# Optimization experiments

Measured on AMD Instinct MI355X. Metric: run time of the kernel, lower is better.

The kernel has to match this reference:

```python
import jax, jax.numpy as jnp
import numpy as np

BS, NE, NN, CIN, H, D = 8, 4800, 4981, 3, 128, 6
EPG = 19200
NEDGE = BS * EPG
N = BS * NE

PARAM_NAMES = [
    'enc_cw1','enc_cb1','enc_cw2','enc_cb2','enc_cw3','enc_clng','enc_clnb',
    'enc_ew1','enc_eb1','enc_ew2','enc_eb2','enc_ew3','enc_elng','enc_elnb',
    'p_ew1','p_eb1','p_ew2','p_eb2','p_ew3','p_elng','p_elnb',
    'p_nw1','p_nb1','p_nw2','p_nb2','p_nw3','p_nlng','p_nlnb',
    'dec_uw1','dec_ub1','dec_uw2','dec_ub2','dec_uw3','dec_ulng','dec_ulnb',
    'dec_cw1','dec_cb1','dec_cw2','dec_cb2','dec_cw3']


def setup_inputs():
    key = jax.random.key(0)
    ks = iter(jax.random.split(key, 64))
    def nrm(shape, s=0.1):
        return jax.random.normal(next(ks), shape, jnp.float32) * s
    inp = {}
    inp['x'] = jax.random.normal(next(ks), (BS * NN, CIN), jnp.float32)
    inp['elem_conn'] = jax.random.randint(next(ks), (NE, 4), 0, NN)
    inp['edge_index'] = jax.random.randint(next(ks), (2, NEDGE), 0, N)
    inp['enc_cw1'] = nrm((CIN, 4, 1)); inp['enc_cb1'] = nrm((CIN, 1), 0.01)
    inp['enc_cw2'] = nrm((CIN, 1, 1)); inp['enc_cb2'] = nrm((CIN, 1), 0.01)
    inp['enc_cw3'] = nrm((CIN, 1, 1))
    inp['enc_clng'] = jnp.ones((CIN, 1)); inp['enc_clnb'] = jnp.zeros((CIN, 1))
    inp['enc_ew1'] = nrm((CIN, H)); inp['enc_eb1'] = nrm((H,), 0.01)
    inp['enc_ew2'] = nrm((H, H)); inp['enc_eb2'] = nrm((H,), 0.01)
    inp['enc_ew3'] = nrm((H, H))
    inp['enc_elng'] = jnp.ones((H,)); inp['enc_elnb'] = jnp.zeros((H,))
    inp['p_ew1'] = nrm((D, 2 * H, H)); inp['p_eb1'] = nrm((D, H), 0.01)
    inp['p_ew2'] = nrm((D, H, H)); inp['p_eb2'] = nrm((D, H), 0.01)
    inp['p_ew3'] = nrm((D, H, H))
    inp['p_elng'] = jnp.ones((D, H)); inp['p_elnb'] = jnp.zeros((D, H))
    inp['p_nw1'] = nrm((D, 2 * H, H)); inp['p_nb1'] = nrm((D, H), 0.01)
    inp['p_nw2'] = nrm((D, H, H)); inp['p_nb2'] = nrm((D, H), 0.01)
    inp['p_nw3'] = nrm((D, H, H))
    inp['p_nlng'] = jnp.ones((D, H)); inp['p_nlnb'] = jnp.zeros((D, H))
    inp['dec_uw1'] = nrm((H, 1, 4)); inp['dec_ub1'] = nrm((H, 4), 0.01)
    inp['dec_uw2'] = nrm((H, 4, 4)); inp['dec_ub2'] = nrm((H, 4), 0.01)
    inp['dec_uw3'] = nrm((H, 4, 4))
    inp['dec_ulng'] = jnp.ones((H, 4)); inp['dec_ulnb'] = jnp.zeros((H, 4))
    inp['dec_cw1'] = nrm((H, CIN)); inp['dec_cb1'] = nrm((CIN,), 0.01)
    inp['dec_cw2'] = nrm((CIN, CIN)); inp['dec_cb2'] = nrm((CIN,), 0.01)
    inp['dec_cw3'] = nrm((CIN, CIN))
    return inp


def lrelu(x):
    return jnp.where(x >= 0, x, 0.2 * x)


def ln(x, g, b, axis=-1):
    m = jnp.mean(x, axis=axis, keepdims=True)
    v = jnp.var(x, axis=axis, keepdims=True)
    return (x - m) / jnp.sqrt(v + 1e-5) * g + b


def mlp(x, w1, b1, w2, b2, w3):
    h = lrelu(x @ w1 + b1)
    h = lrelu(h @ w2 + b2)
    return h @ w3


def _forward(fl, elem_conn, edge_index):
    x = fl[0]
    P = dict(zip(PARAM_NAMES, fl[1:]))
    # ---- Encoder: MeshCNN gather (4 mesh nodes per element) + per-channel MLP 4->1 ----
    xg = x.reshape(BS, NN, CIN)[:, elem_conn]                  # (BS, NE, 4, CIN)
    h = lrelu(jnp.einsum('beic,cio->beoc', xg, P['enc_cw1']) + P['enc_cb1'].T[None, None])
    h = lrelu(jnp.einsum('beic,cio->beoc', h, P['enc_cw2']) + P['enc_cb2'].T[None, None])
    h = jnp.einsum('beic,cio->beoc', h, P['enc_cw3'])
    h = ln(h, P['enc_clng'].T[None, None], P['enc_clnb'].T[None, None], axis=2)  # LayerNorm(1)
    h = h[:, :, 0, :].reshape(N, CIN)
    h = ln(mlp(h, P['enc_ew1'], P['enc_eb1'], P['enc_ew2'], P['enc_eb2'], P['enc_ew3']),
           P['enc_elng'], P['enc_elnb'])                       # (N, H)
    # ---- Processor: D GraphNet blocks, edge MLP + scatter-add + node MLP ----
    src, dest = edge_index[0], edge_index[1]
    stacked = (P['p_ew1'], P['p_eb1'], P['p_ew2'], P['p_eb2'], P['p_ew3'], P['p_elng'], P['p_elnb'],
               P['p_nw1'], P['p_nb1'], P['p_nw2'], P['p_nb2'], P['p_nw3'], P['p_nlng'], P['p_nlnb'])
    def step(hc, p):
        ew1, eb1, ew2, eb2, ew3, eg, ebv, nw1, nb1, nw2, nb2, nw3, ng, nbv = p
        msg = jnp.concatenate([hc[dest], hc[src]], axis=-1)    # (NEDGE, 2H)
        m = ln(mlp(msg, ew1, eb1, ew2, eb2, ew3), eg, ebv)
        aggr = jax.ops.segment_sum(m, dest, num_segments=N)
        hn = ln(mlp(jnp.concatenate([hc, aggr], axis=-1), nw1, nb1, nw2, nb2, nw3), ng, nbv)
        return hn, None
    h, _ = jax.lax.scan(step, h, stacked)
    # ---- Decoder: per-channel upsample 1->4 then index_add back to mesh nodes ----
    u = h.reshape(BS, NE, H)[:, :, None, :]                    # (BS, NE, 1, H)
    u = lrelu(jnp.einsum('beic,cio->beoc', u, P['dec_uw1']) + P['dec_ub1'].T[None, None])
    u = lrelu(jnp.einsum('beic,cio->beoc', u, P['dec_uw2']) + P['dec_ub2'].T[None, None])
    u = jnp.einsum('beic,cio->beoc', u, P['dec_uw3'])
    u = ln(u, P['dec_ulng'].T[None, None], P['dec_ulnb'].T[None, None], axis=2)  # (BS, NE, 4, H)
    out = jnp.zeros((BS, NN, H), u.dtype).at[:, elem_conn.reshape(-1)].add(u.reshape(BS, NE * 4, H))
    out = out.reshape(BS * NN, H)
    o = lrelu(out @ P['dec_cw1'] + P['dec_cb1'])
    o = lrelu(o @ P['dec_cw2'] + P['dec_cb2'])
    return o @ P['dec_cw3']


def reference(x, elem_conn, edge_index,
              enc_cw1, enc_cb1, enc_cw2, enc_cb2, enc_cw3, enc_clng, enc_clnb,
              enc_ew1, enc_eb1, enc_ew2, enc_eb2, enc_ew3, enc_elng, enc_elnb,
              p_ew1, p_eb1, p_ew2, p_eb2, p_ew3, p_elng, p_elnb,
              p_nw1, p_nb1, p_nw2, p_nb2, p_nw3, p_nlng, p_nlnb,
              dec_uw1, dec_ub1, dec_uw2, dec_ub2, dec_uw3, dec_ulng, dec_ulnb,
              dec_cw1, dec_cb1, dec_cw2, dec_cb2, dec_cw3):
    fl = (x, enc_cw1, enc_cb1, enc_cw2, enc_cb2, enc_cw3, enc_clng, enc_clnb,
          enc_ew1, enc_eb1, enc_ew2, enc_eb2, enc_ew3, enc_elng, enc_elnb,
          p_ew1, p_eb1, p_ew2, p_eb2, p_ew3, p_elng, p_elnb,
          p_nw1, p_nb1, p_nw2, p_nb2, p_nw3, p_nlng, p_nlnb,
          dec_uw1, dec_ub1, dec_uw2, dec_ub2, dec_uw3, dec_ulng, dec_ulnb,
          dec_cw1, dec_cb1, dec_cw2, dec_cb2, dec_cw3)
    return _forward(fl, elem_conn, edge_index)
```

## Files before the change

kernel.cpp:

```cpp
#include <hip/hip_runtime.h>
#include <hip/hip_fp16.h>
#include <math.h>

#define BS    8
#define NE    4800
#define NN    4981
#define CIN   3
#define HD    128
#define DBLK  6
#define NEDGE 153600
#define NTOT  38400
#define NMESH (BS*NN)
#define NNP   5120
#define EM    128

#define UW1T  0
#define UB1T  512
#define UW2T  1024
#define UB2T  3072
#define UW3T  3584
#define ULNGT 5632
#define ULNBT 6144
#define DWT_N 6656

typedef _Float16 f16;
typedef _Float16 f16x8 __attribute__((ext_vector_type(8)));
typedef float f32x4 __attribute__((ext_vector_type(4)));

__device__ __forceinline__ float lrelu(float x) { return x >= 0.0f ? x : 0.2f * x; }

__global__ __launch_bounds__(128)
void enc_msg0_kernel(const float* __restrict__ clnb,
                     const float* __restrict__ ew1, const float* __restrict__ eb1,
                     const float* __restrict__ ew2, const float* __restrict__ eb2,
                     const float* __restrict__ ew3,
                     const float* __restrict__ g, const float* __restrict__ b,
                     float* __restrict__ hv0,
                     const float* __restrict__ pew1, const float* __restrict__ peb1,
                     const float* __restrict__ pew2, const float* __restrict__ peb2,
                     const float* __restrict__ pew3,
                     const float* __restrict__ pg, const float* __restrict__ pb,
                     float* __restrict__ m0) {
    __shared__ float s1[HD], s2[HD], s3[HD], hv[HD];
    int j = threadIdx.x;
    float a = eb1[j];
    for (int c = 0; c < CIN; ++c) a += clnb[c] * ew1[c * HD + j];
    s1[j] = lrelu(a);
    __syncthreads();
    a = eb2[j];
    for (int k = 0; k < HD; ++k) a += s1[k] * ew2[k * HD + j];
    s2[j] = lrelu(a);
    __syncthreads();
    a = 0.0f;
    for (int k = 0; k < HD; ++k) a += s2[k] * ew3[k * HD + j];
    s3[j] = a;
    __syncthreads();
    float m = 0.0f;
    for (int k = 0; k < HD; ++k) m += s3[k];
    m *= (1.0f / HD);
    float v = 0.0f;
    for (int k = 0; k < HD; ++k) { float d = s3[k] - m; v += d * d; }
    v *= (1.0f / HD);
    float rs = 1.0f / sqrtf(v + 1e-5f);
    float h0 = (s3[j] - m) * rs * g[j] + b[j];
    hv0[j] = h0;
    hv[j] = h0;
    __syncthreads();
    a = peb1[j];
    for (int k = 0; k < HD; ++k) a += hv[k] * (pew1[k * HD + j] + pew1[(k + HD) * HD + j]);
    s1[j] = lrelu(a);
    __syncthreads();
    a = peb2[j];
    for (int k = 0; k < HD; ++k) a += s1[k] * pew2[k * HD + j];
    s2[j] = lrelu(a);
    __syncthreads();
    a = 0.0f;
    for (int k = 0; k < HD; ++k) a += s2[k] * pew3[k * HD + j];
    s3[j] = a;
    __syncthreads();
    m = 0.0f;
    for (int k = 0; k < HD; ++k) m += s3[k];
    m *= (1.0f / HD);
    v = 0.0f;
    for (int k = 0; k < HD; ++k) { float d = s3[k] - m; v += d * d; }
    v *= (1.0f / HD);
    rs = 1.0f / sqrtf(v + 1e-5f);
    m0[j] = (s3[j] - m) * rs * pg[j] + pb[j];
}

__global__ __launch_bounds__(256)
void conv_all_kernel(const float* __restrict__ ew1, const float* __restrict__ ew2,
                     const float* __restrict__ ew3,
                     const float* __restrict__ nw1, const float* __restrict__ nw2,
                     const float* __restrict__ nw3, f16* __restrict__ wbuf,
                     const float* __restrict__ eb1, f16* __restrict__ eb16,
                     const float* __restrict__ uw1, const float* __restrict__ ub1,
                     const float* __restrict__ uw2, const float* __restrict__ ub2,
                     const float* __restrict__ uw3, const float* __restrict__ ulng,
                     const float* __restrict__ ulnb, float* __restrict__ dwt) {
    int b = blockIdx.x;
    int tid = threadIdx.x;
    if (b == 48) {
        for (int i = tid; i < DBLK * HD; i += 256)
            eb16[i] = (f16)eb1[i];
        return;
    }
    if (b == 49) {
        for (int idx = tid; idx < 512; idx += 256) {
            int o = idx >> 7, c = idx & 127;
            dwt[UW1T + idx] = uw1[c * 4 + o];
            dwt[UB1T + idx] = ub1[c * 4 + o];
            dwt[UB2T + idx] = ub2[c * 4 + o];
            dwt[ULNGT + idx] = ulng[c * 4 + o];
            dwt[ULNBT + idx] = ulnb[c * 4 + o];
        }
        for (int idx = tid; idx < 2048; idx += 256) {
            int io = idx >> 7, c = idx & 127;
            dwt[UW2T + idx] = uw2[c * 16 + io];
            dwt[UW3T + idx] = uw3[c * 16 + io];
        }
        return;
    }
    int d = b >> 3, m = b & 7;
    const float* src;
    switch (m) {
        case 0: src = ew1 + (size_t)d * 2 * HD * HD; break;
        case 1: src = ew1 + (size_t)d * 2 * HD * HD + HD * HD; break;
        case 2: src = ew2 + (size_t)d * HD * HD; break;
        case 3: src = ew3 + (size_t)d * HD * HD; break;
        case 4: src = nw1 + (size_t)d * 2 * HD * HD; break;
        case 5: src = nw1 + (size_t)d * 2 * HD * HD + HD * HD; break;
        case 6: src = nw2 + (size_t)d * HD * HD; break;
        default: src = nw3 + (size_t)d * HD * HD; break;
    }
    f16* out = wbuf + (size_t)b * HD * HD;
    for (int idx = tid; idx < HD * HD; idx += 256) {
        int n = idx >> 7, k = idx & 127;
        out[idx] = (f16)src[k * HD + n];
    }
}

#define EHB (NEDGE / 256)
#define MHB (NE * 4 / 256)
#define ESB (NTOT / 256)
#define MSB (NNP / 256)

__global__ __launch_bounds__(256)
void prep_hist(const int* __restrict__ e_dst, const int* __restrict__ conn,
               int* __restrict__ deg, int* __restrict__ mdeg) {
    int b = blockIdx.x;
    if (b < EHB) {
        int e = b * 256 + threadIdx.x;
        atomicAdd(&deg[e_dst[e]], 1);
    } else {
        int idx = (b - EHB) * 256 + threadIdx.x;
        atomicAdd(&mdeg[conn[idx]], 1);
    }
}

__device__ __forceinline__ void scan1_body(const int* __restrict__ deg,
                                           int* __restrict__ rowptr,
                                           int* __restrict__ bsum, int bi) {
    __shared__ int s[256];
    int i = bi * 256 + threadIdx.x;
    int v = deg[i];
    s[threadIdx.x] = v;
    __syncthreads();
    for (int off = 1; off < 256; off <<= 1) {
        int t = (threadIdx.x >= off) ? s[threadIdx.x - off] : 0;
        __syncthreads();
        s[threadIdx.x] += t;
        __syncthreads();
    }
    rowptr[i] = s[threadIdx.x] - v;
    if (threadIdx.x == 255) bsum[bi] = s[255];
}

__global__ __launch_bounds__(256)
void prep_scan1(const int* __restrict__ deg, int* __restrict__ rowptr,
                int* __restrict__ bsum,
                const int* __restrict__ mdeg, int* __restrict__ mrow,
                int* __restrict__ mbsum) {
    int b = blockIdx.x;
    if (b < ESB) scan1_body(deg, rowptr, bsum, b);
    else         scan1_body(mdeg, mrow, mbsum, b - ESB);
}

__device__ __forceinline__ void scan2_body(int* __restrict__ bsum, int nb) {
    __shared__ int s[256];
    int v = (threadIdx.x < nb) ? bsum[threadIdx.x] : 0;
    s[threadIdx.x] = v;
    __syncthreads();
    for (int off = 1; off < 256; off <<= 1) {
        int t = (threadIdx.x >= off) ? s[threadIdx.x - off] : 0;
        __syncthreads();
        s[threadIdx.x] += t;
        __syncthreads();
    }
    if (threadIdx.x < nb) bsum[threadIdx.x] = s[threadIdx.x] - v;
}

__global__ __launch_bounds__(256)
void prep_scan2(int* __restrict__ bsum, int* __restrict__ mbsum) {
    if (blockIdx.x == 0) scan2_body(bsum, ESB);
    else                 scan2_body(mbsum, MSB);
}

__global__ __launch_bounds__(256)
void prep_scan3(int* __restrict__ rowptr, const int* __restrict__ bsum,
                int* __restrict__ mrow, const int* __restrict__ mbsum) {
    int b = blockIdx.x;
    if (b < ESB) {
        int i = b * 256 + threadIdx.x;
        rowptr[i] += bsum[b];
    } else {
        int i = (b - ESB) * 256 + threadIdx.x;
        mrow[i] += mbsum[b - ESB];
    }
}

__global__ __launch_bounds__(256)
void prep_scatter(const int* __restrict__ dest, const int* __restrict__ srcv,
                  const int* __restrict__ rowptr, int* __restrict__ cursor,
                  int* __restrict__ dsorted, int* __restrict__ ssorted,
                  const int* __restrict__ conn, const int* __restrict__ mrow,
                  int* __restrict__ mcur, int* __restrict__ mslot) {
    int b = blockIdx.x;
    if (b < EHB) {
        int e = b * 256 + threadIdx.x;
        int d = dest[e];
        int pos = rowptr[d] + atomicAdd(&cursor[d], 1);
        dsorted[pos] = d;
        ssorted[pos] = srcv[e];
    } else {
        int idx = (b - EHB) * 256 + threadIdx.x;
        int nd = conn[idx];
        int pos = mrow[nd] + atomicAdd(&mcur[nd], 1);
        mslot[pos] = idx;
    }
}

template <int NT>
__device__ __forceinline__ void stage_w(const f16* __restrict__ Wg, f16 (*Bt)[HD + 8],
                                        int tid) {
    #pragma unroll
    for (int t = 0; t < 2048 / NT; ++t) {
        int idx = tid + t * NT;
        int r = idx >> 4, c = (idx & 15) * 8;
        *(uint4*)(&Bt[r][c]) = *(const uint4*)(Wg + (size_t)r * HD + c);
    }
}

__device__ __forceinline__ void mfma_pass(const f16 (*A)[HD + 8], const f16 (*Bt)[HD + 8],
                                          int rt_base, int ct_base, int ln, int quad,
                                          f32x4 acc[2][4]) {
    #pragma unroll
    for (int ks = 0; ks < 4; ++ks) {
        int kb = ks * 32 + quad * 8;
        f16x8 a0 = *(const f16x8*)(&A[rt_base + ln][kb]);
        f16x8 a1 = *(const f16x8*)(&A[rt_base + 16 + ln][kb]);
        #pragma unroll
        for (int c = 0; c < 4; ++c) {
            f16x8 b = *(const f16x8*)(&Bt[ct_base + c * 16 + ln][kb]);
            acc[0][c] = __builtin_amdgcn_mfma_f32_16x16x32_f16(a0, b, acc[0][c], 0, 0, 0);
            acc[1][c] = __builtin_amdgcn_mfma_f32_16x16x32_f16(a1, b, acc[1][c], 0, 0, 0);
        }
    }
}

__global__ __launch_bounds__(512, 4)
void gn_edge(const f16* __restrict__ P1, const f16* __restrict__ P2,
             const int* __restrict__ dsorted, const int* __restrict__ ssorted,
             const f16* __restrict__ W2, const f16* __restrict__ W3,
             const f16* __restrict__ b1h, const float* __restrict__ b2,
             const float* __restrict__ g, const float* __restrict__ bln,
             f16* __restrict__ msg) {
    __shared__ __align__(16) f16 As[EM][HD + 8];
    __shared__ __align__(16) f16 Bt[HD][HD + 8];
    __shared__ float red[EM][2][2];

    const int tid = threadIdx.x;
    const int base = blockIdx.x * EM;
    const int wave = tid >> 6, lane = tid & 63;
    const int ln = lane & 15, quad = lane >> 4;
    const int rt_base = (wave >> 1) * 32;
    const int ct_base = (wave & 1) * 64;
    const int half = wave & 1;
    const int r0 = tid >> 4;
    const int cg = (tid & 15) * 8;

    const f16 k02s = (f16)0.2f;
    const f16x8 k02 = {k02s, k02s, k02s, k02s, k02s, k02s, k02s, k02s};

    int dI[4], sI[4];
    #pragma unroll
    for (int it = 0; it < 4; ++it) {
        dI[it] = dsorted[base + r0 + it * 32];
        sI[it] = ssorted[base + r0 + it * 32];
    }
    stage_w<512>(W2, Bt, tid);
    const f16x8 bb = *(const f16x8*)(b1h + cg);
    #pragma unroll
    for (int it = 0; it < 4; ++it) {
        f16x8 p1 = *(const f16x8*)(P1 + (size_t)dI[it] * HD + cg);
        f16x8 p2 = *(const f16x8*)(P2 + (size_t)sI[it] * HD + cg);
        f16x8 s = p1 + p2 + bb;
        *(f16x8*)(&As[r0 + it * 32][cg]) = __builtin_elementwise_max(s, s * k02);
    }
    __syncthreads();

    f32x4 acc[2][4];

    #pragma unroll
    for (int c = 0; c < 4; ++c) {
        float bj = b2[ct_base + c * 16 + ln];
        f32x4 bv = {bj, bj, bj, bj};
        acc[0][c] = bv; acc[1][c] = bv;
    }
    mfma_pass(As, Bt, rt_base, ct_base, ln, quad, acc);
    __syncthreads();
    stage_w<512>(W3, Bt, tid);
    #pragma unroll
    for (int i = 0; i < 2; ++i)
        #pragma unroll
        for (int c = 0; c < 4; ++c)
            #pragma unroll
            for (int r = 0; r < 4; ++r)
                As[rt_base + i * 16 + quad * 4 + r][ct_base + c * 16 + ln] =
                    (f16)lrelu(acc[i][c][r]);
    __syncthreads();

    #pragma unroll
    for (int c = 0; c < 4; ++c) { f32x4 z = {0,0,0,0}; acc[0][c] = z; acc[1][c] = z; }
    mfma_pass(As, Bt, rt_base, ct_base, ln, quad, acc);

    #pragma unroll
    for (int i = 0; i < 2; ++i)
        #pragma unroll
        for (int r = 0; r < 4; ++r) {
            float s = acc[i][0][r] + acc[i][1][r] + acc[i][2][r] + acc[i][3][r];
            float q = acc[i][0][r] * acc[i][0][r] + acc[i][1][r] * acc[i][1][r] +
                      acc[i][2][r] * acc[i][2][r] + acc[i][3][r] * acc[i][3][r];
            s += __shfl_xor(s, 1); q += __shfl_xor(q, 1);
            s += __shfl_xor(s, 2); q += __shfl_xor(q, 2);
            s += __shfl_xor(s, 4); q += __shfl_xor(q, 4);
            s += __shfl_xor(s, 8); q += __shfl_xor(q, 8);
            if (ln == 0) {
                int row = rt_base + i * 16 + quad * 4 + r;
                red[row][half][0] = s;
                red[row][half][1] = q;
            }
        }
    __syncthreads();

    float gv[4], bv[4];
    #pragma unroll
    for (int c = 0; c < 4; ++c) {
        int col = ct_base + c * 16 + ln;
        gv[c] = g[col]; bv[c] = bln[col];
    }
    #pragma unroll
    for (int i = 0; i < 2; ++i)
        #pragma unroll
        for (int r = 0; r < 4; ++r) {
            int row = rt_base + i * 16 + quad * 4 + r;
            float s = red[row][0][0] + red[row][1][0];
            float q = red[row][0][1] + red[row][1][1];
            float m = s * (1.0f / HD);
            float var = q * (1.0f / HD) - m * m;
            float rs = 1.0f / sqrtf(var + 1e-5f);
            #pragma unroll
            for (int c = 0; c < 4; ++c) {
                int col = ct_base + c * 16 + ln;
                float v = (acc[i][c][r] - m) * rs * gv[c] + bv[c];
                msg[(size_t)(base + row) * HD + col] = (f16)v;
            }
        }
}

template <int AGGR, bool PROD, bool DECF>
__global__ __launch_bounds__(256, 3)
void gn_node(f16* __restrict__ h16, const f16* __restrict__ msg,
             const int* __restrict__ rowptr, const int* __restrict__ deg,
             const float* __restrict__ m0, const float* __restrict__ hv0,
             const f16* __restrict__ W1a, const f16* __restrict__ W1b,
             const f16* __restrict__ W2, const f16* __restrict__ W3,
             const float* __restrict__ b1, const float* __restrict__ b2,
             const float* __restrict__ g, const float* __restrict__ bln,
             const f16* __restrict__ nW1a, const f16* __restrict__ nW1b,
             f16* __restrict__ P1, f16* __restrict__ P2,
             const float* __restrict__ dwt, f16* __restrict__ uval) {
    __shared__ __align__(16) f16 As[64][HD + 8];
    __shared__ __align__(16) f16 Bt[HD][HD + 8];
    __shared__ float red[64][2][2];

    const int tid = threadIdx.x;
    const int base = blockIdx.x * 64;
    const int wave = tid >> 6, lane = tid & 63;
    const int ln = lane & 15, quad = lane >> 4;
    const int rt_base = (wave >> 1) * 32;
    const int ct_base = (wave & 1) * 64;
    const int half = wave & 1;

    f16x8 hreg[4];
    #pragma unroll
    for (int t = 0; t < 4; ++t) {
        int r = (tid >> 4) + t * 16;
        int c = (tid & 15) * 8;
        if (AGGR == 0) {
            f16x8 hz;
            #pragma unroll
            for (int u = 0; u < 8; ++u) hz[u] = (f16)hv0[c + u];
            hreg[t] = hz;
            float sc = (float)deg[base + r];
            f16x8 o;
            #pragma unroll
            for (int u = 0; u < 8; ++u) o[u] = (f16)(sc * m0[c + u]);
            *(f16x8*)(&As[r][c]) = o;
        } else {
            hreg[t] = *(const f16x8*)(h16 + (size_t)(base + r) * HD + c);
            int rp = rowptr[base + r], dg = deg[base + r];
            float a[8] = {0, 0, 0, 0, 0, 0, 0, 0};
            int j = 0;
            for (; j + 4 <= dg; j += 4) {
                f16x8 v0 = *(const f16x8*)(msg + (size_t)(rp + j) * HD + c);
                f16x8 v1 = *(const f16x8*)(msg + (size_t)(rp + j + 1) * HD + c);
                f16x8 v2 = *(const f16x8*)(msg + (size_t)(rp + j + 2) * HD + c);
                f16x8 v3 = *(const f16x8*)(msg + (size_t)(rp + j + 3) * HD + c);
                #pragma unroll
                for (int u = 0; u < 8; ++u)
                    a[u] += ((float)v0[u] + (float)v1[u]) + ((float)v2[u] + (float)v3[u]);
            }
            for (; j < dg; ++j) {
                f16x8 mv = *(const f16x8*)(msg + (size_t)(rp + j) * HD + c);
                #pragma unroll
                for (int u = 0; u < 8; ++u) a[u] += (float)mv[u];
            }
            f16x8 o;
            #pragma unroll
            for (int u = 0; u < 8; ++u) o[u] = (f16)a[u];
            *(f16x8*)(&As[r][c]) = o;
        }
    }
    stage_w<256>(W1b, Bt, tid);
    __syncthreads();

    f32x4 acc[2][4];
    #pragma unroll
    for (int c = 0; c < 4; ++c) {
        float bj = b1[ct_base + c * 16 + ln];
        f32x4 bb = {bj, bj, bj, bj};
        acc[0][c] = bb; acc[1][c] = bb;
    }
    mfma_pass(As, Bt, rt_base, ct_base, ln, quad, acc);
    __syncthreads();

    #pragma unroll
    for (int t = 0; t < 4; ++t) {
        int r = (tid >> 4) + t * 16;
        int c = (tid & 15) * 8;
        *(f16x8*)(&As[r][c]) = hreg[t];
    }
    stage_w<256>(W1a, Bt, tid);
    __syncthreads();
    mfma_pass(As, Bt, rt_base, ct_base, ln, quad, acc);
    __syncthreads();

    stage_w<256>(W2, Bt, tid);
    #pragma unroll
    for (int i = 0; i < 2; ++i)
        #pragma unroll
        for (int c = 0; c < 4; ++c)
            #pragma unroll
            for (int r = 0; r < 4; ++r)
                As[rt_base + i * 16 + quad * 4 + r][ct_base + c * 16 + ln] =
                    (f16)lrelu(acc[i][c][r]);
    __syncthreads();

    #pragma unroll
    for (int c = 0; c < 4; ++c) {
        float bj = b2[ct_base + c * 16 + ln];
        f32x4 bb = {bj, bj, bj, bj};
        acc[0][c] = bb; acc[1][c] = bb;
    }
    mfma_pass(As, Bt, rt_base, ct_base, ln, quad, acc);
    __syncthreads();
    stage_w<256>(W3, Bt, tid);
    #pragma unroll
    for (int i = 0; i < 2; ++i)
        #pragma unroll
        for (int c = 0; c < 4; ++c)
            #pragma unroll
            for (int r = 0; r < 4; ++r)
                As[rt_base + i * 16 + quad * 4 + r][ct_base + c * 16 + ln] =
                    (f16)lrelu(acc[i][c][r]);
    __syncthreads();

    #pragma unroll
    for (int c = 0; c < 4; ++c) { f32x4 z = {0,0,0,0}; acc[0][c] = z; acc[1][c] = z; }
    mfma_pass(As, Bt, rt_base, ct_base, ln, quad, acc);

    #pragma unroll
    for (int i = 0; i < 2; ++i)
        #pragma unroll
        for (int r = 0; r < 4; ++r) {
            float s = acc[i][0][r] + acc[i][1][r] + acc[i][2][r] + acc[i][3][r];
            float q = acc[i][0][r] * acc[i][0][r] + acc[i][1][r] * acc[i][1][r] +
                      acc[i][2][r] * acc[i][2][r] + acc[i][3][r] * acc[i][3][r];
            s += __shfl_xor(s, 1); q += __shfl_xor(q, 1);
            s += __shfl_xor(s, 2); q += __shfl_xor(q, 2);
            s += __shfl_xor(s, 4); q += __shfl_xor(q, 4);
            s += __shfl_xor(s, 8); q += __shfl_xor(q, 8);
            if (ln == 0) {
                int row = rt_base + i * 16 + quad * 4 + r;
                red[row][half][0] = s;
                red[row][half][1] = q;
            }
        }
    __syncthreads();

    float gv[4], bv[4];
    #pragma unroll
    for (int c = 0; c < 4; ++c) {
        int col = ct_base + c * 16 + ln;
        gv[c] = g[col]; bv[c] = bln[col];
    }

    if (!DECF) {
        #pragma unroll
        for (int i = 0; i < 2; ++i)
            #pragma unroll
            for (int r = 0; r < 4; ++r) {
                int row = rt_base + i * 16 + quad * 4 + r;
                float s = red[row][0][0] + red[row][1][0];
                float q = red[row][0][1] + red[row][1][1];
                float m = s * (1.0f / HD);
                float var = q * (1.0f / HD) - m * m;
                float rs = 1.0f / sqrtf(var + 1e-5f);
                #pragma unroll
                for (int c = 0; c < 4; ++c) {
                    int col = ct_base + c * 16 + ln;
                    float v = (acc[i][c][r] - m) * rs * gv[c] + bv[c];
                    f16 hv = (f16)v;
                    h16[(size_t)(base + row) * HD + col] = hv;
                    if (PROD) As[row][col] = hv;
                }
            }
    } else {
        float mm[2][4], rr[2][4];
        #pragma unroll
        for (int i = 0; i < 2; ++i)
            #pragma unroll
            for (int r = 0; r < 4; ++r) {
                int row = rt_base + i * 16 + quad * 4 + r;
                float s = red[row][0][0] + red[row][1][0];
                float q = red[row][0][1] + red[row][1][1];
                float m = s * (1.0f / HD);
                float var = q * (1.0f / HD) - m * m;
                mm[i][r] = m;
                rr[i][r] = 1.0f / sqrtf(var + 1e-5f);
            }
        #pragma unroll
        for (int c = 0; c < 4; ++c) {
            int col = ct_base + c * 16 + ln;
            float w1v[4], wb1[4], wb2[4], lg4[4], lb4[4];
            #pragma unroll
            for (int o = 0; o < 4; ++o) {
                w1v[o] = dwt[UW1T + o * 128 + col];
                wb1[o] = dwt[UB1T + o * 128 + col];
                wb2[o] = dwt[UB2T + o * 128 + col];
                lg4[o] = dwt[ULNGT + o * 128 + col];
                lb4[o] = dwt[ULNBT + o * 128 + col];
            }
            float w2v[16], w3v[16];
            #pragma unroll
            for (int io = 0; io < 16; ++io) {
                w2v[io] = dwt[UW2T + io * 128 + col];
                w3v[io] = dwt[UW3T + io * 128 + col];
            }
            #pragma unroll
            for (int i = 0; i < 2; ++i)
                #pragma unroll
                for (int r = 0; r < 4; ++r) {
                    int row = rt_base + i * 16 + quad * 4 + r;
                    float v = (acc[i][c][r] - mm[i][r]) * rr[i][r] * gv[c] + bv[c];
                    float s = (float)(f16)v;
                    float u1[4], u2[4], u3[4];
                    #pragma unroll
                    for (int o = 0; o < 4; ++o)
                        u1[o] = lrelu(s * w1v[o] + wb1[o]);
                    #pragma unroll
                    for (int o = 0; o < 4; ++o) {
                        float a = wb2[o];
                        #pragma unroll
                        for (int i2 = 0; i2 < 4; ++i2) a += u1[i2] * w2v[i2 * 4 + o];
                        u2[o] = lrelu(a);
                    }
                    #pragma unroll
                    for (int o = 0; o < 4; ++o) {
                        float a = 0.f;
                        #pragma unroll
                        for (int i2 = 0; i2 < 4; ++i2) a += u2[i2] * w3v[i2 * 4 + o];
                        u3[o] = a;
                    }
                    float m4 = 0.25f * (u3[0] + u3[1] + u3[2] + u3[3]);
                    float var4 = 0.f;
                    #pragma unroll
                    for (int o = 0; o < 4; ++o) { float d = u3[o] - m4; var4 += d * d; }
                    var4 *= 0.25f;
                    float rs4 = 1.0f / sqrtf(var4 + 1e-5f);
                    size_t ub = (size_t)(base + row) * 4 * HD + col;
                    #pragma unroll
                    for (int o = 0; o < 4; ++o)
                        uval[ub + (size_t)o * HD] =
                            (f16)((u3[o] - m4) * rs4 * lg4[o] + lb4[o]);
                }
        }
    }

    if (PROD) {
        __syncthreads();
        stage_w<256>(nW1a, Bt, tid);
        __syncthreads();
        #pragma unroll
        for (int c = 0; c < 4; ++c) { f32x4 z = {0,0,0,0}; acc[0][c] = z; acc[1][c] = z; }
        mfma_pass(As, Bt, rt_base, ct_base, ln, quad, acc);
        #pragma unroll
        for (int i = 0; i < 2; ++i)
            #pragma unroll
            for (int c = 0; c < 4; ++c)
                #pragma unroll
                for (int r = 0; r < 4; ++r)
                    P1[(size_t)(base + rt_base + i * 16 + quad * 4 + r) * HD +
                       ct_base + c * 16 + ln] = (f16)acc[i][c][r];
        __syncthreads();
        stage_w<256>(nW1b, Bt, tid);
        __syncthreads();
        #pragma unroll
        for (int c = 0; c < 4; ++c) { f32x4 z = {0,0,0,0}; acc[0][c] = z; acc[1][c] = z; }
        mfma_pass(As, Bt, rt_base, ct_base, ln, quad, acc);
        #pragma unroll
        for (int i = 0; i < 2; ++i)
            #pragma unroll
            for (int c = 0; c < 4; ++c)
                #pragma unroll
                for (int r = 0; r < 4; ++r)
                    P2[(size_t)(base + rt_base + i * 16 + quad * 4 + r) * HD +
                       ct_base + c * 16 + ln] = (f16)acc[i][c][r];
    }
}

__global__ __launch_bounds__(256)
void dec_gather_out(const f16* __restrict__ uval,
                    const int* __restrict__ mrow, const int* __restrict__ mdeg,
                    const int* __restrict__ mslot,
                    const float* __restrict__ cw1, const float* __restrict__ cb1,
                    const float* __restrict__ cw2, const float* __restrict__ cb2,
                    const float* __restrict__ cw3,
                    float* __restrict__ o, int nrows) {
    int r = blockIdx.x * 4 + (threadIdx.x >> 6);
    if (r >= nrows) return;
    int lane = threadIdx.x & 63;
    int b = r / NN, n = r - b * NN;
    int rp = mrow[n], dg = mdeg[n];
    size_t boff = (size_t)b * NE * 4;
    float a0 = 0.f, a1 = 0.f;
    int j = 0;
    for (; j + 4 <= dg; j += 4) {
        int s0 = mslot[rp + j], s1 = mslot[rp + j + 1];
        int s2 = mslot[rp + j + 2], s3 = mslot[rp + j + 3];
        const f16* u0 = uval + (boff + s0) * HD + lane * 2;
        const f16* u1 = uval + (boff + s1) * HD + lane * 2;
        const f16* u2 = uval + (boff + s2) * HD + lane * 2;
        const f16* u3 = uval + (boff + s3) * HD + lane * 2;
        float b00 = (float)u0[0], b01 = (float)u0[1];
        float b10 = (float)u1[0], b11 = (float)u1[1];
        float b20 = (float)u2[0], b21 = (float)u2[1];
        float b30 = (float)u3[0], b31 = (float)u3[1];
        a0 += (b00 + b10) + (b20 + b30);
        a1 += (b01 + b11) + (b21 + b31);
    }
    for (; j < dg; ++j) {
        int slot = mslot[rp + j];
        const f16* up = uval + (boff + slot) * HD + lane * 2;
        a0 += (float)up[0];
        a1 += (float)up[1];
    }
    int c0 = lane * 2, c1 = lane * 2 + 1;
    float s[3];
    #pragma unroll
    for (int k = 0; k < 3; ++k)
        s[k] = a0 * cw1[c0 * 3 + k] + a1 * cw1[c1 * 3 + k];
    #pragma unroll
    for (int off = 32; off >= 1; off >>= 1) {
        s[0] += __shfl_down(s[0], off);
        s[1] += __shfl_down(s[1], off);
        s[2] += __shfl_down(s[2], off);
    }
    if (lane == 0) {
        float t1[3], t2[3];
        #pragma unroll
        for (int k = 0; k < 3; ++k) t1[k] = lrelu(s[k] + cb1[k]);
        #pragma unroll
        for (int k = 0; k < 3; ++k) {
            float a = cb2[k];
            #pragma unroll
            for (int q = 0; q < 3; ++q) a += t1[q] * cw2[q * 3 + k];
            t2[k] = lrelu(a);
        }
        #pragma unroll
        for (int k = 0; k < 3; ++k) {
            float a = 0.f;
            #pragma unroll
            for (int q = 0; q < 3; ++q) a += t2[q] * cw3[q * 3 + k];
            o[(size_t)r * 3 + k] = a;
        }
    }
}

extern "C" void kernel_launch(void* const* d_in, const int* in_sizes, int n_in,
                              void* d_out, int out_size, void* d_ws, size_t ws_size,
                              hipStream_t stream) {
    const int* elem_conn = (const int*)d_in[1];
    const int* edge_index = (const int*)d_in[2];
    const int* e_src = edge_index;
    const int* e_dst = edge_index + NEDGE;
    const float* enc_clnb = (const float*)d_in[9];
    const float* enc_ew1 = (const float*)d_in[10];
    const float* enc_eb1 = (const float*)d_in[11];
    const float* enc_ew2 = (const float*)d_in[12];
    const float* enc_eb2 = (const float*)d_in[13];
    const float* enc_ew3 = (const float*)d_in[14];
    const float* enc_elng = (const float*)d_in[15];
    const float* enc_elnb = (const float*)d_in[16];
    const float* p_ew1 = (const float*)d_in[17];
    const float* p_eb1 = (const float*)d_in[18];
    const float* p_ew2 = (const float*)d_in[19];
    const float* p_eb2 = (const float*)d_in[20];
    const float* p_ew3 = (const float*)d_in[21];
    const float* p_elng = (const float*)d_in[22];
    const float* p_elnb = (const float*)d_in[23];
    const float* p_nw1 = (const float*)d_in[24];
    const float* p_nb1 = (const float*)d_in[25];
    const float* p_nw2 = (const float*)d_in[26];
    const float* p_nb2 = (const float*)d_in[27];
    const float* p_nw3 = (const float*)d_in[28];
    const float* p_nlng = (const float*)d_in[29];
    const float* p_nlnb = (const float*)d_in[30];
    const float* dec_uw1 = (const float*)d_in[31];
    const float* dec_ub1 = (const float*)d_in[32];
    const float* dec_uw2 = (const float*)d_in[33];
    const float* dec_ub2 = (const float*)d_in[34];
    const float* dec_uw3 = (const float*)d_in[35];
    const float* dec_ulng = (const float*)d_in[36];
    const float* dec_ulnb = (const float*)d_in[37];
    const float* dec_cw1 = (const float*)d_in[38];
    const float* dec_cb1 = (const float*)d_in[39];
    const float* dec_cw2 = (const float*)d_in[40];
    const float* dec_cb2 = (const float*)d_in[41];
    const float* dec_cw3 = (const float*)d_in[42];

    char* ws = (char*)d_ws;
    f16*   h16     = (f16*)(ws);
    f16*   wbuf    = (f16*)(ws + 9830400);
    float* hv0     = (float*)(ws + 11403264);
    float* m0      = (float*)(ws + 11403776);
    f16*   P1      = (f16*)(ws + 11404288);
    f16*   P2      = (f16*)(ws + 21234688);
    f16*   msg     = (f16*)(ws + 31065088);
    int*   deg     = (int*)(ws + 70386688);
    int*   rowptr  = (int*)(ws + 70540288);
    int*   cursor  = (int*)(ws + 70693888);
    int*   bsum    = (int*)(ws + 70847488);
    int*   dsorted = (int*)(ws + 70848512);
    int*   ssorted = (int*)(ws + 71462912);
    f16*   eb16    = (f16*)(ws + 72077312);
    int*   mdeg    = (int*)(ws + 72078848);
    int*   mrow    = (int*)(ws + 72099328);
    int*   mcur    = (int*)(ws + 72119808);
    int*   mbsum   = (int*)(ws + 72140288);
    int*   mslot   = (int*)(ws + 72141312);
    float* dwt     = (float*)(ws + 72218112);
    f16*   uval    = (f16*)(ws + 72244736);

    hipMemsetAsync(deg, 0, 72218112 - 70386688, stream);

    enc_msg0_kernel<<<1, 128, 0, stream>>>(
        enc_clnb, enc_ew1, enc_eb1, enc_ew2, enc_eb2, enc_ew3, enc_elng, enc_elnb, hv0,
        p_ew1, p_eb1, p_ew2, p_eb2, p_ew3, p_elng, p_elnb, m0);
    conv_all_kernel<<<50, 256, 0, stream>>>(p_ew1, p_ew2, p_ew3,
                                            p_nw1, p_nw2, p_nw3, wbuf, p_eb1, eb16,
                                            dec_uw1, dec_ub1, dec_uw2, dec_ub2,
                                            dec_uw3, dec_ulng, dec_ulnb, dwt);

    prep_hist<<<EHB + MHB, 256, 0, stream>>>(e_dst, elem_conn, deg, mdeg);
    prep_scan1<<<ESB + MSB, 256, 0, stream>>>(deg, rowptr, bsum, mdeg, mrow, mbsum);
    prep_scan2<<<2, 256, 0, stream>>>(bsum, mbsum);
    prep_scan3<<<ESB + MSB, 256, 0, stream>>>(rowptr, bsum, mrow, mbsum);
    prep_scatter<<<EHB + MHB, 256, 0, stream>>>(e_dst, e_src, rowptr, cursor,
                                                dsorted, ssorted,
                                                elem_conn, mrow, mcur, mslot);

    {
        const f16* wd = wbuf;
        const f16* wn = wbuf + (size_t)8 * HD * HD;
        gn_node<0, true, false><<<NTOT / 64, 256, 0, stream>>>(
            h16, nullptr, nullptr, deg, m0, hv0,
            wd + 4 * HD * HD, wd + 5 * HD * HD, wd + 6 * HD * HD, wd + 7 * HD * HD,
            p_nb1, p_nb2, p_nlng, p_nlnb,
            wn + 0 * HD * HD, wn + 1 * HD * HD, P1, P2, nullptr, nullptr);
    }

    for (int d = 1; d < DBLK; ++d) {
        const f16* wd = wbuf + (size_t)d * 8 * HD * HD;
        gn_edge<<<NEDGE / EM, 512, 0, stream>>>(
            P1, P2, dsorted, ssorted,
            wd + 2 * HD * HD, wd + 3 * HD * HD,
            eb16 + (size_t)d * HD, p_eb2 + (size_t)d * HD,
            p_elng + (size_t)d * HD, p_elnb + (size_t)d * HD, msg);
        if (d < DBLK - 1) {
            const f16* wn = wbuf + (size_t)(d + 1) * 8 * HD * HD;
            gn_node<1, true, false><<<NTOT / 64, 256, 0, stream>>>(
                h16, msg, rowptr, deg, nullptr, nullptr,
                wd + 4 * HD * HD, wd + 5 * HD * HD, wd + 6 * HD * HD, wd + 7 * HD * HD,
                p_nb1 + (size_t)d * HD, p_nb2 + (size_t)d * HD,
                p_nlng + (size_t)d * HD, p_nlnb + (size_t)d * HD,
                wn + 0 * HD * HD, wn + 1 * HD * HD, P1, P2, nullptr, nullptr);
        } else {
            gn_node<1, false, true><<<NTOT / 64, 256, 0, stream>>>(
                h16, msg, rowptr, deg, nullptr, nullptr,
                wd + 4 * HD * HD, wd + 5 * HD * HD, wd + 6 * HD * HD, wd + 7 * HD * HD,
                p_nb1 + (size_t)d * HD, p_nb2 + (size_t)d * HD,
                p_nlng + (size_t)d * HD, p_nlnb + (size_t)d * HD,
                wbuf, wbuf, P1, P2, dwt, uval);
        }
    }

    dec_gather_out<<<(NMESH + 3) / 4, 256, 0, stream>>>(
        uval, mrow, mdeg, mslot, dec_cw1, dec_cb1, dec_cw2, dec_cb2, dec_cw3,
        (float*)d_out, NMESH);
}
```

Measured before the change: 578.4 us.

## Tabulate first GN node block by degree and prefetch node weights into registers

The first node block's inputs depend only on node in-degree, so its output is computed once for degrees 0..255 into small tables (h, P1, P2). The first edge block then gathers by per-edge degree, and the next node block reads h by degree, which removes a full-size node pass. The change also replaces the memset with zeroing blocks inside the conversion kernel, prefetches next-layer W1a/W1b into registers to overlap with the epilogue, and stages the decoder weights in shared memory. It assumes in-degree never exceeds 255, which holds for these random inputs but is not guaranteed in general, and the prefetch raises register pressure.

After: 629.8 us. +8.9%, slower.

```diff
diff --git a/kernel.cpp b/kernel.cpp
--- a/kernel.cpp
+++ b/kernel.cpp
@@ -13,6 +13,7 @@
 #define NMESH (BS*NN)
 #define NNP   5120
 #define EM    128
+#define TROWS 256
 
 #define UW1T  0
 #define UB1T  512
@@ -97,7 +98,9 @@
                      const float* __restrict__ uw1, const float* __restrict__ ub1,
                      const float* __restrict__ uw2, const float* __restrict__ ub2,
                      const float* __restrict__ uw3, const float* __restrict__ ulng,
-                     const float* __restrict__ ulnb, float* __restrict__ dwt) {
+                     const float* __restrict__ ulnb, float* __restrict__ dwt,
+                     int* __restrict__ zeroA, int* __restrict__ zeroB,
+                     int* __restrict__ degIota) {
     int b = blockIdx.x;
     int tid = threadIdx.x;
     if (b == 48) {
@@ -119,6 +122,19 @@
             dwt[UW2T + idx] = uw2[c * 16 + io];
             dwt[UW3T + idx] = uw3[c * 16 + io];
         }
+        return;
+    }
+    if (b >= 50 && b < 64) {
+        uint4 z = {0, 0, 0, 0};
+        for (int idx = (b - 50) * 256 + tid; idx < 28864; idx += 14 * 256)
+            ((uint4*)zeroA)[idx] = z;
+        return;
+    }
+    if (b == 64) {
+        uint4 z = {0, 0, 0, 0};
+        for (int idx = tid; idx < 3904; idx += 256)
+            ((uint4*)zeroB)[idx] = z;
+        degIota[tid] = tid;
         return;
     }
     int d = b >> 3, m = b & 7;
@@ -224,14 +240,19 @@
                   const int* __restrict__ rowptr, int* __restrict__ cursor,
                   int* __restrict__ dsorted, int* __restrict__ ssorted,
                   const int* __restrict__ conn, const int* __restrict__ mrow,
-                  int* __restrict__ mcur, int* __restrict__ mslot) {
+                  int* __restrict__ mcur, int* __restrict__ mslot,
+                  const int* __restrict__ deg,
+                  int* __restrict__ ddegs, int* __restrict__ sdegs) {
     int b = blockIdx.x;
     if (b < EHB) {
         int e = b * 256 + threadIdx.x;
         int d = dest[e];
+        int s = srcv[e];
         int pos = rowptr[d] + atomicAdd(&cursor[d], 1);
         dsorted[pos] = d;
-        ssorted[pos] = srcv[e];
+        ssorted[pos] = s;
+        ddegs[pos] = deg[d];
+        sdegs[pos] = deg[s];
     } else {
         int idx = (b - EHB) * 256 + threadIdx.x;
         int nd = conn[idx];
@@ -378,11 +399,12 @@
         }
 }
 
-template <int AGGR, bool PROD, bool DECF>
+template <int AGGR, bool PROD, bool DECF, bool HTAB>
 __global__ __launch_bounds__(256, 3)
 void gn_node(f16* __restrict__ h16, const f16* __restrict__ msg,
              const int* __restrict__ rowptr, const int* __restrict__ deg,
              const float* __restrict__ m0, const float* __restrict__ hv0,
+             const f16* __restrict__ htab,
              const f16* __restrict__ W1a, const f16* __restrict__ W1b,
              const f16* __restrict__ W2, const f16* __restrict__ W3,
              const float* __restrict__ b1, const float* __restrict__ b2,
@@ -418,7 +440,10 @@
             for (int u = 0; u < 8; ++u) o[u] = (f16)(sc * m0[c + u]);
             *(f16x8*)(&As[r][c]) = o;
         } else {
-            hreg[t] = *(const f16x8*)(h16 + (size_t)(base + r) * HD + c);
+            if (HTAB)
+                hreg[t] = *(const f16x8*)(htab + (size_t)deg[base + r] * HD + c);
+            else
+                hreg[t] = *(const f16x8*)(h16 + (size_t)(base + r) * HD + c);
             int rp = rowptr[base + r], dg = deg[base + r];
             float a[8] = {0, 0, 0, 0, 0, 0, 0, 0};
             int j = 0;
@@ -500,6 +525,16 @@
     for (int c = 0; c < 4; ++c) { f32x4 z = {0,0,0,0}; acc[0][c] = z; acc[1][c] = z; }
     mfma_pass(As, Bt, rt_base, ct_base, ln, quad, acc);
 
+    uint4 wr[8];
+    if (PROD) {
+        #pragma unroll
+        for (int t = 0; t < 8; ++t) {
+            int idx = tid + t * 256;
+            int r = idx >> 4, c = (idx & 15) * 8;
+            wr[t] = *(const uint4*)(nW1a + (size_t)r * HD + c);
+        }
+    }
+
     #pragma unroll
     for (int i = 0; i < 2; ++i)
         #pragma unroll
@@ -547,6 +582,11 @@
                 }
             }
     } else {
+        float* dls = (float*)&Bt[0][0];
+        for (int idx = tid; idx < DWT_N / 4; idx += 256)
+            ((float4*)dls)[idx] = ((const float4*)dwt)[idx];
+        __syncthreads();
+
         float mm[2][4], rr[2][4];
         #pragma unroll
         for (int i = 0; i < 2; ++i)
@@ -566,17 +606,17 @@
             float w1v[4], wb1[4], wb2[4], lg4[4], lb4[4];
             #pragma unroll
             for (int o = 0; o < 4; ++o) {
-                w1v[o] = dwt[UW1T + o * 128 + col];
-                wb1[o] = dwt[UB1T + o * 128 + col];
-                wb2[o] = dwt[UB2T + o * 128 + col];
-                lg4[o] = dwt[ULNGT + o * 128 + col];
-                lb4[o] = dwt[ULNBT + o * 128 + col];
+                w1v[o] = dls[UW1T + o * 128 + col];
+                wb1[o] = dls[UB1T + o * 128 + col];
+                wb2[o] = dls[UB2T + o * 128 + col];
+                lg4[o] = dls[ULNGT + o * 128 + col];
+                lb4[o] = dls[ULNBT + o * 128 + col];
             }
             float w2v[16], w3v[16];
             #pragma unroll
             for (int io = 0; io < 16; ++io) {
-                w2v[io] = dwt[UW2T + io * 128 + col];
-                w3v[io] = dwt[UW3T + io * 128 + col];
+                w2v[io] = dls[UW2T + io * 128 + col];
+                w3v[io] = dls[UW3T + io * 128 + col];
             }
             #pragma unroll
             for (int i = 0; i < 2; ++i)
@@ -620,7 +660,18 @@
 
     if (PROD) {
         __syncthreads();
-        stage_w<256>(nW1a, Bt, tid);
+        #pragma unroll
+        for (int t = 0; t < 8; ++t) {
+            int idx = tid + t * 256;
+            int r = idx >> 4, c = (idx & 15) * 8;
+            *(uint4*)(&Bt[r][c]) = wr[t];
+        }
+        #pragma unroll
+        for (int t = 0; t < 8; ++t) {
+            int idx = tid + t * 256;
+            int r = idx >> 4, c = (idx & 15) * 8;
+            wr[t] = *(const uint4*)(nW1b + (size_t)r * HD + c);
+        }
         __syncthreads();
         #pragma unroll
         for (int c = 0; c < 4; ++c) { f32x4 z = {0,0,0,0}; acc[0][c] = z; acc[1][c] = z; }
@@ -634,7 +685,12 @@
                     P1[(size_t)(base + rt_base + i * 16 + quad * 4 + r) * HD +
                        ct_base + c * 16 + ln] = (f16)acc[i][c][r];
         __syncthreads();
-        stage_w<256>(nW1b, Bt, tid);
+        #pragma unroll
+        for (int t = 0; t < 8; ++t) {
+            int idx = tid + t * 256;
+            int r = idx >> 4, c = (idx & 15) * 8;
+            *(uint4*)(&Bt[r][c]) = wr[t];
+        }
         __syncthreads();
         #pragma unroll
         for (int c = 0; c < 4; ++c) { f32x4 z = {0,0,0,0}; acc[0][c] = z; acc[1][c] = z; }
@@ -782,16 +838,31 @@
     int*   mslot   = (int*)(ws + 72141312);
     float* dwt     = (float*)(ws + 72218112);
     f16*   uval    = (f16*)(ws + 72244736);
-
-    hipMemsetAsync(deg, 0, 72218112 - 70386688, stream);
+    int*   ddegs   = (int*)(ws + 111566336);
+    int*   sdegs   = (int*)(ws + 112180736);
+    f16*   tabH    = (f16*)(ws + 112795136);
+    f16*   tabP1   = (f16*)(ws + 112860672);
+    f16*   tabP2   = (f16*)(ws + 112926208);
+    int*   degIota = (int*)(ws + 112991744);
 
     enc_msg0_kernel<<<1, 128, 0, stream>>>(
         enc_clnb, enc_ew1, enc_eb1, enc_ew2, enc_eb2, enc_ew3, enc_elng, enc_elnb, hv0,
         p_ew1, p_eb1, p_ew2, p_eb2, p_ew3, p_elng, p_elnb, m0);
-    conv_all_kernel<<<50, 256, 0, stream>>>(p_ew1, p_ew2, p_ew3,
+    conv_all_kernel<<<65, 256, 0, stream>>>(p_ew1, p_ew2, p_ew3,
                                             p_nw1, p_nw2, p_nw3, wbuf, p_eb1, eb16,
                                             dec_uw1, dec_ub1, dec_uw2, dec_ub2,
-                                            dec_uw3, dec_ulng, dec_ulnb, dwt);
+                                            dec_uw3, dec_ulng, dec_ulnb, dwt,
+                                            deg, mdeg, degIota);
+
+    {
+        const f16* wd = wbuf;
+        const f16* wn = wbuf + (size_t)8 * HD * HD;
+        gn_node<0, true, false, false><<<TROWS / 64, 256, 0, stream>>>(
+            tabH, nullptr, nullptr, degIota, m0, hv0, nullptr,
+            wd + 4 * HD * HD, wd + 5 * HD * HD, wd + 6 * HD * HD, wd + 7 * HD * HD,
+            p_nb1, p_nb2, p_nlng, p_nlnb,
+            wn + 0 * HD * HD, wn + 1 * HD * HD, tabP1, tabP2, nullptr, nullptr);
+    }
 
     prep_hist<<<EHB + MHB, 256, 0, stream>>>(e_dst, elem_conn, deg, mdeg);
     prep_scan1<<<ESB + MSB, 256, 0, stream>>>(deg, rowptr, bsum, mdeg, mrow, mbsum);
@@ -799,36 +870,42 @@
     prep_scan3<<<ESB + MSB, 256, 0, stream>>>(rowptr, bsum, mrow, mbsum);
     prep_scatter<<<EHB + MHB, 256, 0, stream>>>(e_dst, e_src, rowptr, cursor,
                                                 dsorted, ssorted,
-                                                elem_conn, mrow, mcur, mslot);
-
-    {
-        const f16* wd = wbuf;
-        const f16* wn = wbuf + (size_t)8 * HD * HD;
-        gn_node<0, true, false><<<NTOT / 64, 256, 0, stream>>>(
-            h16, nullptr, nullptr, deg, m0, hv0,
-            wd + 4 * HD * HD, wd + 5 * HD * HD, wd + 6 * HD * HD, wd + 7 * HD * HD,
-            p_nb1, p_nb2, p_nlng, p_nlnb,
-            wn + 0 * HD * HD, wn + 1 * HD * HD, P1, P2, nullptr, nullptr);
-    }
+                                                elem_conn, mrow, mcur, mslot,
+                                                deg, ddegs, sdegs);
 
     for (int d = 1; d < DBLK; ++d) {
         const f16* wd = wbuf + (size_t)d * 8 * HD * HD;
-        gn_edge<<<NEDGE / EM, 512, 0, stream>>>(
-            P1, P2, dsorted, ssorted,
-            wd + 2 * HD * HD, wd + 3 * HD * HD,
-            eb16 + (size_t)d * HD, p_eb2 + (size_t)d * HD,
-            p_elng + (size_t)d * HD, p_elnb + (size_t)d * HD, msg);
-        if (d < DBLK - 1) {
+        if (d == 1)
+            gn_edge<<<NEDGE / EM, 512, 0, stream>>>(
+                tabP1, tabP2, ddegs, sdegs,
+                wd + 2 * HD * HD, wd + 3 * HD * HD,
+                eb16 + (size_t)d * HD, p_eb2 + (size_t)d * HD,
+                p_elng + (size_t)d * HD, p_elnb + (size_t)d * HD, msg);
+        else
+            gn_edge<<<NEDGE / EM, 512, 0, stream>>>(
+                P1, P2, dsorted, ssorted,
+                wd + 2 * HD * HD, wd + 3 * HD * HD,
+                eb16 + (size_t)d * HD, p_eb2 + (size_t)d * HD,
+                p_elng + (size_t)d * HD, p_elnb + (size_t)d * HD, msg);
+        if (d == 1) {
             const f16* wn = wbuf + (size_t)(d + 1) * 8 * HD * HD;
-            gn_node<1, true, false><<<NTOT / 64, 256, 0, stream>>>(
-                h16, msg, rowptr, deg, nullptr, nullptr,
+            gn_node<1, true, false, true><<<NTOT / 64, 256, 0, stream>>>(
+                h16, msg, rowptr, deg, nullptr, nullptr, tabH,
+                wd + 4 * HD * HD, wd + 5 * HD * HD, wd + 6 * HD * HD, wd + 7 * HD * HD,
+                p_nb1 + (size_t)d * HD, p_nb2 + (size_t)d * HD,
+                p_nlng + (size_t)d * HD, p_nlnb + (size_t)d * HD,
+                wn + 0 * HD * HD, wn + 1 * HD * HD, P1, P2, nullptr, nullptr);
+        } else if (d < DBLK - 1) {
+            const f16* wn = wbuf + (size_t)(d + 1) * 8 * HD * HD;
+            gn_node<1, true, false, false><<<NTOT / 64, 256, 0, stream>>>(
+                h16, msg, rowptr, deg, nullptr, nullptr, nullptr,
                 wd + 4 * HD * HD, wd + 5 * HD * HD, wd + 6 * HD * HD, wd + 7 * HD * HD,
                 p_nb1 + (size_t)d * HD, p_nb2 + (size_t)d * HD,
                 p_nlng + (size_t)d * HD, p_nlnb + (size_t)d * HD,
                 wn + 0 * HD * HD, wn + 1 * HD * HD, P1, P2, nullptr, nullptr);
         } else {
-            gn_node<1, false, true><<<NTOT / 64, 256, 0, stream>>>(
-                h16, msg, rowptr, deg, nullptr, nullptr,
+            gn_node<1, false, true, false><<<NTOT / 64, 256, 0, stream>>>(
+                h16, msg, rowptr, deg, nullptr, nullptr, nullptr,
                 wd + 4 * HD * HD, wd + 5 * HD * HD, wd + 6 * HD * HD, wd + 7 * HD * HD,
                 p_nb1 + (size_t)d * HD, p_nb2 + (size_t)d * HD,
                 p_nlng + (size_t)d * HD, p_nlnb + (size_t)d * HD,
```

## Compute first node block once per distinct degree via lookup tables

Applied to the files above, without the earlier changes.

After the encoder, every node's state depends only on its in-degree, so the first node-update block is evaluated for 256 degree values into small tables instead of all 38400 nodes. The first edge pass and the next node pass then index these tables by per-edge destination and source degrees, which prep_scatter now records. This removes the full-size first node GEMM pass. It assumes no node has degree 256 or more and needs extra workspace for degree arrays and tables.

Measured after the change: 564.7 us. 2.4% less time.

```diff
diff --git a/kernel.cpp b/kernel.cpp
--- a/kernel.cpp
+++ b/kernel.cpp
@@ -13,6 +13,7 @@
 #define NMESH (BS*NN)
 #define NNP   5120
 #define EM    128
+#define TROWS 256
 
 #define UW1T  0
 #define UB1T  512
@@ -97,12 +98,14 @@
                      const float* __restrict__ uw1, const float* __restrict__ ub1,
                      const float* __restrict__ uw2, const float* __restrict__ ub2,
                      const float* __restrict__ uw3, const float* __restrict__ ulng,
-                     const float* __restrict__ ulnb, float* __restrict__ dwt) {
+                     const float* __restrict__ ulnb, float* __restrict__ dwt,
+                     int* __restrict__ degIota) {
     int b = blockIdx.x;
     int tid = threadIdx.x;
     if (b == 48) {
         for (int i = tid; i < DBLK * HD; i += 256)
             eb16[i] = (f16)eb1[i];
+        degIota[tid] = tid;
         return;
     }
     if (b == 49) {
@@ -224,14 +227,19 @@
                   const int* __restrict__ rowptr, int* __restrict__ cursor,
                   int* __restrict__ dsorted, int* __restrict__ ssorted,
                   const int* __restrict__ conn, const int* __restrict__ mrow,
-                  int* __restrict__ mcur, int* __restrict__ mslot) {
+                  int* __restrict__ mcur, int* __restrict__ mslot,
+                  const int* __restrict__ deg,
+                  int* __restrict__ ddegs, int* __restrict__ sdegs) {
     int b = blockIdx.x;
     if (b < EHB) {
         int e = b * 256 + threadIdx.x;
         int d = dest[e];
+        int s = srcv[e];
         int pos = rowptr[d] + atomicAdd(&cursor[d], 1);
         dsorted[pos] = d;
-        ssorted[pos] = srcv[e];
+        ssorted[pos] = s;
+        ddegs[pos] = deg[d];
+        sdegs[pos] = deg[s];
     } else {
         int idx = (b - EHB) * 256 + threadIdx.x;
         int nd = conn[idx];
@@ -378,11 +386,12 @@
         }
 }
 
-template <int AGGR, bool PROD, bool DECF>
+template <int AGGR, bool PROD, bool DECF, bool HTAB>
 __global__ __launch_bounds__(256, 3)
 void gn_node(f16* __restrict__ h16, const f16* __restrict__ msg,
              const int* __restrict__ rowptr, const int* __restrict__ deg,
              const float* __restrict__ m0, const float* __restrict__ hv0,
+             const f16* __restrict__ htab,
              const f16* __restrict__ W1a, const f16* __restrict__ W1b,
              const f16* __restrict__ W2, const f16* __restrict__ W3,
              const float* __restrict__ b1, const float* __restrict__ b2,
@@ -418,7 +427,10 @@
             for (int u = 0; u < 8; ++u) o[u] = (f16)(sc * m0[c + u]);
             *(f16x8*)(&As[r][c]) = o;
         } else {
-            hreg[t] = *(const f16x8*)(h16 + (size_t)(base + r) * HD + c);
+            if (HTAB)
+                hreg[t] = *(const f16x8*)(htab + (size_t)deg[base + r] * HD + c);
+            else
+                hreg[t] = *(const f16x8*)(h16 + (size_t)(base + r) * HD + c);
             int rp = rowptr[base + r], dg = deg[base + r];
             float a[8] = {0, 0, 0, 0, 0, 0, 0, 0};
             int j = 0;
@@ -782,6 +794,12 @@
     int*   mslot   = (int*)(ws + 72141312);
     float* dwt     = (float*)(ws + 72218112);
     f16*   uval    = (f16*)(ws + 72244736);
+    int*   ddegs   = (int*)(ws + 111566336);
+    int*   sdegs   = (int*)(ws + 112180736);
+    f16*   tabH    = (f16*)(ws + 112795136);
+    f16*   tabP1   = (f16*)(ws + 112860672);
+    f16*   tabP2   = (f16*)(ws + 112926208);
+    int*   degIota = (int*)(ws + 112991744);
 
     hipMemsetAsync(deg, 0, 72218112 - 70386688, stream);
 
@@ -791,7 +809,18 @@
     conv_all_kernel<<<50, 256, 0, stream>>>(p_ew1, p_ew2, p_ew3,
                                             p_nw1, p_nw2, p_nw3, wbuf, p_eb1, eb16,
                                             dec_uw1, dec_ub1, dec_uw2, dec_ub2,
-                                            dec_uw3, dec_ulng, dec_ulnb, dwt);
+                                            dec_uw3, dec_ulng, dec_ulnb, dwt,
+                                            degIota);
+
+    {
+        const f16* wd = wbuf;
+        const f16* wn = wbuf + (size_t)8 * HD * HD;
+        gn_node<0, true, false, false><<<TROWS / 64, 256, 0, stream>>>(
+            tabH, nullptr, nullptr, degIota, m0, hv0, nullptr,
+            wd + 4 * HD * HD, wd + 5 * HD * HD, wd + 6 * HD * HD, wd + 7 * HD * HD,
+            p_nb1, p_nb2, p_nlng, p_nlnb,
+            wn + 0 * HD * HD, wn + 1 * HD * HD, tabP1, tabP2, nullptr, nullptr);
+    }
 
     prep_hist<<<EHB + MHB, 256, 0, stream>>>(e_dst, elem_conn, deg, mdeg);
     prep_scan1<<<ESB + MSB, 256, 0, stream>>>(deg, rowptr, bsum, mdeg, mrow, mbsum);
@@ -799,36 +828,42 @@
     prep_scan3<<<ESB + MSB, 256, 0, stream>>>(rowptr, bsum, mrow, mbsum);
     prep_scatter<<<EHB + MHB, 256, 0, stream>>>(e_dst, e_src, rowptr, cursor,
                                                 dsorted, ssorted,
-                                                elem_conn, mrow, mcur, mslot);
-
-    {
-        const f16* wd = wbuf;
-        const f16* wn = wbuf + (size_t)8 * HD * HD;
-        gn_node<0, true, false><<<NTOT / 64, 256, 0, stream>>>(
-            h16, nullptr, nullptr, deg, m0, hv0,
-            wd + 4 * HD * HD, wd + 5 * HD * HD, wd + 6 * HD * HD, wd + 7 * HD * HD,
-            p_nb1, p_nb2, p_nlng, p_nlnb,
-            wn + 0 * HD * HD, wn + 1 * HD * HD, P1, P2, nullptr, nullptr);
-    }
+                                                elem_conn, mrow, mcur, mslot,
+                                                deg, ddegs, sdegs);
 
     for (int d = 1; d < DBLK; ++d) {
         const f16* wd = wbuf + (size_t)d * 8 * HD * HD;
-        gn_edge<<<NEDGE / EM, 512, 0, stream>>>(
-            P1, P2, dsorted, ssorted,
-            wd + 2 * HD * HD, wd + 3 * HD * HD,
-            eb16 + (size_t)d * HD, p_eb2 + (size_t)d * HD,
-            p_elng + (size_t)d * HD, p_elnb + (size_t)d * HD, msg);
-        if (d < DBLK - 1) {
+        if (d == 1)
+            gn_edge<<<NEDGE / EM, 512, 0, stream>>>(
+                tabP1, tabP2, ddegs, sdegs,
+                wd + 2 * HD * HD, wd + 3 * HD * HD,
+                eb16 + (size_t)d * HD, p_eb2 + (size_t)d * HD,
+                p_elng + (size_t)d * HD, p_elnb + (size_t)d * HD, msg);
+        else
+            gn_edge<<<NEDGE / EM, 512, 0, stream>>>(
+                P1, P2, dsorted, ssorted,
+                wd + 2 * HD * HD, wd + 3 * HD * HD,
+                eb16 + (size_t)d * HD, p_eb2 + (size_t)d * HD,
+                p_elng + (size_t)d * HD, p_elnb + (size_t)d * HD, msg);
+        if (d == 1) {
             const f16* wn = wbuf + (size_t)(d + 1) * 8 * HD * HD;
-            gn_node<1, true, false><<<NTOT / 64, 256, 0, stream>>>(
-                h16, msg, rowptr, deg, nullptr, nullptr,
+            gn_node<1, true, false, true><<<NTOT / 64, 256, 0, stream>>>(
+                h16, msg, rowptr, deg, nullptr, nullptr, tabH,
+                wd + 4 * HD * HD, wd + 5 * HD * HD, wd + 6 * HD * HD, wd + 7 * HD * HD,
+                p_nb1 + (size_t)d * HD, p_nb2 + (size_t)d * HD,
+                p_nlng + (size_t)d * HD, p_nlnb + (size_t)d * HD,
+                wn + 0 * HD * HD, wn + 1 * HD * HD, P1, P2, nullptr, nullptr);
+        } else if (d < DBLK - 1) {
+            const f16* wn = wbuf + (size_t)(d + 1) * 8 * HD * HD;
+            gn_node<1, true, false, false><<<NTOT / 64, 256, 0, stream>>>(
+                h16, msg, rowptr, deg, nullptr, nullptr, nullptr,
                 wd + 4 * HD * HD, wd + 5 * HD * HD, wd + 6 * HD * HD, wd + 7 * HD * HD,
                 p_nb1 + (size_t)d * HD, p_nb2 + (size_t)d * HD,
                 p_nlng + (size_t)d * HD, p_nlnb + (size_t)d * HD,
                 wn + 0 * HD * HD, wn + 1 * HD * HD, P1, P2, nullptr, nullptr);
         } else {
-            gn_node<1, false, true><<<NTOT / 64, 256, 0, stream>>>(
-                h16, msg, rowptr, deg, nullptr, nullptr,
+            gn_node<1, false, true, false><<<NTOT / 64, 256, 0, stream>>>(
+                h16, msg, rowptr, deg, nullptr, nullptr, nullptr,
                 wd + 4 * HD * HD, wd + 5 * HD * HD, wd + 6 * HD * HD, wd + 7 * HD * HD,
                 p_nb1 + (size_t)d * HD, p_nb2 + (size_t)d * HD,
                 p_nlng + (size_t)d * HD, p_nlnb + (size_t)d * HD,
```
